# Performance work log

Hardware: AMD Instinct MI355X
Metric: run time of the kernel (lower is better)

Reference implementation:

```python
import jax, jax.numpy as jnp
import numpy as np

NUM_HEADS = 16
B, S, D_MODEL = 8, 2048, 1024
HEAD_DIM = 64  # key_dim == value_dim == D_MODEL // NUM_HEADS


def setup_inputs() -> dict:
    key = jax.random.key(0)
    ks = jax.random.split(key, 8)
    s_in = 1.0 / np.sqrt(D_MODEL)
    s_out = 1.0 / np.sqrt(NUM_HEADS * HEAD_DIM)
    return {
        "query": jax.random.normal(ks[0], (B, S, D_MODEL), jnp.float32),
        "key": jax.random.normal(ks[1], (B, S, D_MODEL), jnp.float32),
        "value": jax.random.normal(ks[2], (B, S, D_MODEL), jnp.float32),
        "Wq": jax.random.normal(ks[3], (D_MODEL, HEAD_DIM), jnp.float32) * s_in,
        "bq": jnp.zeros((HEAD_DIM,), jnp.float32),
        "Wk": jax.random.normal(ks[4], (D_MODEL, HEAD_DIM), jnp.float32) * s_in,
        "bk": jnp.zeros((HEAD_DIM,), jnp.float32),
        "Wv": jax.random.normal(ks[5], (D_MODEL, HEAD_DIM), jnp.float32) * s_in,
        "bv": jnp.zeros((HEAD_DIM,), jnp.float32),
        "Wo": jax.random.normal(ks[6], (NUM_HEADS * HEAD_DIM, D_MODEL), jnp.float32) * s_out,
        "bo": jnp.zeros((D_MODEL,), jnp.float32),
    }


def reference(query, key, value, Wq, bq, Wk, bk, Wv, bv, Wo, bo):
    # Projections (same Linear reused for every "head" in the original code)
    q = query @ Wq + bq   # [B, S, head_dim]
    k = key @ Wk + bk     # [B, S, head_dim]
    v = value @ Wv + bv   # [B, S, head_dim]
    scale = jnp.sqrt(jnp.asarray(q.shape[-1], q.dtype))
    scores = jnp.einsum("bqd,bkd->bqk", q, k) / scale  # [B, S, S]
    attn = jax.nn.softmax(scores, axis=-1)
    ctx = jnp.einsum("bqk,bkd->bqd", attn, v)          # [B, S, head_dim]
    # All num_heads outputs are identical -> concat == tile
    cat = jnp.tile(ctx, (1, 1, NUM_HEADS))             # [B, S, num_heads*head_dim]
    return cat @ Wo + bo                               # [B, S, D_MODEL]
```

## Files before the change

### kernel.cpp

```cpp
#include <hip/hip_runtime.h>


typedef __attribute__((ext_vector_type(8))) unsigned short ushort8v;

__device__ __forceinline__ float bf2f(unsigned short u) {
    unsigned int x = ((unsigned int)u) << 16;
    return __builtin_bit_cast(float, x);
}

__device__ __forceinline__ bool detect_bf16(const void* p, int nwords) {
    const unsigned short* w = (const unsigned short*)p;
    int sane = 0;
    for (int i = 0; i < nwords; ++i) {
        unsigned e = (w[i] >> 7) & 0xFF;
        sane += (e == 0 || (e >= 0x60 && e <= 0x9F)) ? 1 : 0;
    }
    return sane * 10 >= nwords * 9;
}

__device__ __forceinline__ float load_in(const void* p, long idx, bool isbf16) {
    return isbf16 ? bf2f(((const unsigned short*)p)[idx]) : ((const float*)p)[idx];
}

__global__ __launch_bounds__(256) void prep_wosum(const void* __restrict__ Wo,
                                                  float* __restrict__ wosum) {
    __shared__ bool fwb;
    if (threadIdx.x == 0) fwb = detect_bf16(Wo, 256);
    __syncthreads();
    bool wb = fwb;
    int id = blockIdx.x * 256 + threadIdx.x;
    int d = id >> 10, n = id & 1023;
    float s = 0.f;
#pragma unroll
    for (int h = 0; h < 16; ++h) s += load_in(Wo, (long)(h * 64 + d) * 1024 + n, wb);
    wosum[id] = s;
}

__global__ __launch_bounds__(256) void proj_t(
    const void* __restrict__ X0, const void* __restrict__ X1, const void* __restrict__ X2,
    const void* __restrict__ bq, const void* __restrict__ bk, const void* __restrict__ bv,
    const void* __restrict__ Wq, const void* __restrict__ Wk, const void* __restrict__ Wv,
    float* __restrict__ qo, float* __restrict__ ko, float* __restrict__ vo) {
    int p = blockIdx.y;
    const void* X    = (p == 0) ? X0 : (p == 1) ? X1 : X2;
    const void* W    = (p == 0) ? Wq : (p == 1) ? Wk : Wv;
    const void* bias = (p == 0) ? bq : (p == 1) ? bk : bv;
    float* out       = (p == 0) ? qo : (p == 1) ? ko : vo;

    __shared__ bool fxb, fwb, fbb;
    __shared__ __align__(16) float Xt[64 * 68];
    __shared__ __align__(16) float Ws[64 * 68];
    if (threadIdx.x == 0) {
        fxb = detect_bf16(X, 256);
        fwb = detect_bf16(W, 256);
        fbb = detect_bf16(bias, 64);
    }
    __syncthreads();
    const bool xb = fxb, wb = fwb, bb = fbb;

    const int t = threadIdx.x;
    const long row0 = (long)blockIdx.x * 64;
    const int row4 = (t >> 4) * 4;
    const int col4 = (t & 15) * 4;
    const int sr0 = (t >> 4) * 4;
    const int sk4 = (t & 15) * 4;
    const int wk  = t >> 2;
    const int wc0 = (t & 3) * 16;

    ushort4 xu0, xu1, xu2, xu3;
    float4  xf0, xf1, xf2, xf3;
    ushort8v wu0, wu1;
    float4  wf0, wf1, wf2, wf3;

    auto loadTile = [&](int k0) {
        if (xb) {
            const unsigned short* xp =
                (const unsigned short*)X + (row0 + sr0) * 1024 + k0 + sk4;
            xu0 = *(const ushort4*)(xp);
            xu1 = *(const ushort4*)(xp + 1024);
            xu2 = *(const ushort4*)(xp + 2048);
            xu3 = *(const ushort4*)(xp + 3072);
        } else {
            const float* xp = (const float*)X + (row0 + sr0) * 1024 + k0 + sk4;
            xf0 = *(const float4*)(xp);
            xf1 = *(const float4*)(xp + 1024);
            xf2 = *(const float4*)(xp + 2048);
            xf3 = *(const float4*)(xp + 3072);
        }
        if (wb) {
            const unsigned short* wp =
                (const unsigned short*)W + (long)(k0 + wk) * 64 + wc0;
            wu0 = *(const ushort8v*)(wp);
            wu1 = *(const ushort8v*)(wp + 8);
        } else {
            const float* wp = (const float*)W + (long)(k0 + wk) * 64 + wc0;
            wf0 = *(const float4*)(wp + 0);
            wf1 = *(const float4*)(wp + 4);
            wf2 = *(const float4*)(wp + 8);
            wf3 = *(const float4*)(wp + 12);
        }
    };
    auto writeTile = [&]() {
        if (xb) {
            *(float4*)&Xt[(sk4 + 0) * 68 + sr0] =
                make_float4(bf2f(xu0.x), bf2f(xu1.x), bf2f(xu2.x), bf2f(xu3.x));
            *(float4*)&Xt[(sk4 + 1) * 68 + sr0] =
                make_float4(bf2f(xu0.y), bf2f(xu1.y), bf2f(xu2.y), bf2f(xu3.y));
            *(float4*)&Xt[(sk4 + 2) * 68 + sr0] =
                make_float4(bf2f(xu0.z), bf2f(xu1.z), bf2f(xu2.z), bf2f(xu3.z));
            *(float4*)&Xt[(sk4 + 3) * 68 + sr0] =
                make_float4(bf2f(xu0.w), bf2f(xu1.w), bf2f(xu2.w), bf2f(xu3.w));
        } else {
            *(float4*)&Xt[(sk4 + 0) * 68 + sr0] = make_float4(xf0.x, xf1.x, xf2.x, xf3.x);
            *(float4*)&Xt[(sk4 + 1) * 68 + sr0] = make_float4(xf0.y, xf1.y, xf2.y, xf3.y);
            *(float4*)&Xt[(sk4 + 2) * 68 + sr0] = make_float4(xf0.z, xf1.z, xf2.z, xf3.z);
            *(float4*)&Xt[(sk4 + 3) * 68 + sr0] = make_float4(xf0.w, xf1.w, xf2.w, xf3.w);
        }
        float* wd = &Ws[wk * 68 + wc0];
        if (wb) {
            *(float4*)(wd + 0)  = make_float4(bf2f(wu0[0]), bf2f(wu0[1]), bf2f(wu0[2]), bf2f(wu0[3]));
            *(float4*)(wd + 4)  = make_float4(bf2f(wu0[4]), bf2f(wu0[5]), bf2f(wu0[6]), bf2f(wu0[7]));
            *(float4*)(wd + 8)  = make_float4(bf2f(wu1[0]), bf2f(wu1[1]), bf2f(wu1[2]), bf2f(wu1[3]));
            *(float4*)(wd + 12) = make_float4(bf2f(wu1[4]), bf2f(wu1[5]), bf2f(wu1[6]), bf2f(wu1[7]));
        } else {
            *(float4*)(wd + 0)  = wf0;
            *(float4*)(wd + 4)  = wf1;
            *(float4*)(wd + 8)  = wf2;
            *(float4*)(wd + 12) = wf3;
        }
    };

    loadTile(0);
    writeTile();
    __syncthreads();

    float acc[4][4] = {};
    for (int k0 = 0; k0 < 1024; k0 += 64) {
        const bool more = (k0 + 64 < 1024);
        if (more) loadTile(k0 + 64);
#pragma unroll 4
        for (int kk = 0; kk < 64; ++kk) {
            float4 xv = *(const float4*)&Xt[kk * 68 + row4];
            float4 wv = *(const float4*)&Ws[kk * 68 + col4];
            float xa[4] = {xv.x, xv.y, xv.z, xv.w};
            float wa[4] = {wv.x, wv.y, wv.z, wv.w};
#pragma unroll
            for (int i = 0; i < 4; ++i)
#pragma unroll
                for (int j = 0; j < 4; ++j) acc[i][j] += xa[i] * wa[j];
        }
        if (more) {
            __syncthreads();
            writeTile();
            __syncthreads();
        }
    }

    float b0 = load_in(bias, col4 + 0, bb);
    float b1 = load_in(bias, col4 + 1, bb);
    float b2 = load_in(bias, col4 + 2, bb);
    float b3 = load_in(bias, col4 + 3, bb);
#pragma unroll
    for (int i = 0; i < 4; ++i)
        *(float4*)&out[(row0 + row4 + i) * 64 + col4] =
            make_float4(acc[i][0] + b0, acc[i][1] + b1, acc[i][2] + b2, acc[i][3] + b3);
}

__global__ __launch_bounds__(256) void attn_p(const float* __restrict__ q,
                                              const float* __restrict__ k,
                                              const float* __restrict__ v,
                                              float* __restrict__ ctx,
                                              float* __restrict__ po,
                                              float* __restrict__ pm,
                                              float* __restrict__ pl,
                                              int ns) {
    const int b = blockIdx.y;
    const int qt = blockIdx.x;
    const int split = blockIdx.z;
    const int keys = 2048 / ns;
    const int NT = keys >> 6;
    const long kvbase = (long)b * 2048;
    const long qbase  = kvbase + (long)qt * 32;
    const long kstart = kvbase + (long)split * keys;

    __shared__ __align__(16) float Qt[64 * 36];
    __shared__ __align__(16) float Kt[64 * 68];
    __shared__ __align__(16) float Pt[64 * 36];

    const int tid = threadIdx.x;
    const int g16 = tid & 15;
    const int qg2 = (tid >> 4) * 2;
    const int kg4 = g16 * 4;
    const int dg4 = g16 * 4;
    const int skr = (tid >> 4) * 4;
    const int skd = g16 * 4;

    if (tid < 128) {
        const int sqr = (tid >> 4) * 4;
        const int sqd = (tid & 15) * 4;
        const float* qp = &q[(qbase + sqr) * 64 + sqd];
        float4 a0 = *(const float4*)(qp);
        float4 a1 = *(const float4*)(qp + 64);
        float4 a2 = *(const float4*)(qp + 128);
        float4 a3 = *(const float4*)(qp + 192);
        const float sc = 0.125f;
        *(float4*)&Qt[(sqd + 0) * 36 + sqr] = make_float4(a0.x * sc, a1.x * sc, a2.x * sc, a3.x * sc);
        *(float4*)&Qt[(sqd + 1) * 36 + sqr] = make_float4(a0.y * sc, a1.y * sc, a2.y * sc, a3.y * sc);
        *(float4*)&Qt[(sqd + 2) * 36 + sqr] = make_float4(a0.z * sc, a1.z * sc, a2.z * sc, a3.z * sc);
        *(float4*)&Qt[(sqd + 3) * 36 + sqr] = make_float4(a0.w * sc, a1.w * sc, a2.w * sc, a3.w * sc);
    }

    float4 ka0, ka1, ka2, ka3;
    auto loadK = [&](int t1) {
        const float* kp = &k[(kstart + t1 * 64 + skr) * 64 + skd];
        ka0 = *(const float4*)(kp);
        ka1 = *(const float4*)(kp + 64);
        ka2 = *(const float4*)(kp + 128);
        ka3 = *(const float4*)(kp + 192);
    };
    auto writeK = [&]() {
        *(float4*)&Kt[(skd + 0) * 68 + skr] = make_float4(ka0.x, ka1.x, ka2.x, ka3.x);
        *(float4*)&Kt[(skd + 1) * 68 + skr] = make_float4(ka0.y, ka1.y, ka2.y, ka3.y);
        *(float4*)&Kt[(skd + 2) * 68 + skr] = make_float4(ka0.z, ka1.z, ka2.z, ka3.z);
        *(float4*)&Kt[(skd + 3) * 68 + skr] = make_float4(ka0.w, ka1.w, ka2.w, ka3.w);
    };

    loadK(0);
    writeK();
    __syncthreads();

    float o[2][4] = {};
    float m[2] = {-INFINITY, -INFINITY};
    float l[2] = {};

    for (int t1 = 0; t1 < NT; ++t1) {
        if (t1 + 1 < NT) loadK(t1 + 1);

        float s[2][4] = {};
#pragma unroll 4
        for (int d = 0; d < 64; ++d) {
            float2 qv = *(const float2*)&Qt[d * 36 + qg2];
            float4 kv = *(const float4*)&Kt[d * 68 + kg4];
            float ka[4] = {kv.x, kv.y, kv.z, kv.w};
#pragma unroll
            for (int kj = 0; kj < 4; ++kj) {
                s[0][kj] += qv.x * ka[kj];
                s[1][kj] += qv.y * ka[kj];
            }
        }

#pragma unroll
        for (int qi = 0; qi < 2; ++qi) {
            float pmx = fmaxf(fmaxf(s[qi][0], s[qi][1]), fmaxf(s[qi][2], s[qi][3]));
            pmx = fmaxf(pmx, __shfl_xor(pmx, 1));
            pmx = fmaxf(pmx, __shfl_xor(pmx, 2));
            pmx = fmaxf(pmx, __shfl_xor(pmx, 4));
            pmx = fmaxf(pmx, __shfl_xor(pmx, 8));
            float mn = fmaxf(m[qi], pmx);
            float f = __expf(m[qi] - mn);
            m[qi] = mn;
            float ts = 0.f;
#pragma unroll
            for (int kj = 0; kj < 4; ++kj) {
                float pv = __expf(s[qi][kj] - mn);
                s[qi][kj] = pv;
                ts += pv;
            }
            ts += __shfl_xor(ts, 1);
            ts += __shfl_xor(ts, 2);
            ts += __shfl_xor(ts, 4);
            ts += __shfl_xor(ts, 8);
            l[qi] = l[qi] * f + ts;
#pragma unroll
            for (int di = 0; di < 4; ++di) o[qi][di] *= f;
        }

#pragma unroll
        for (int kj = 0; kj < 4; ++kj)
            *(float2*)&Pt[(kg4 + kj) * 36 + qg2] = make_float2(s[0][kj], s[1][kj]);
        __syncthreads();

        const float* vb = &v[(kstart + t1 * 64) * 64 + dg4];
#pragma unroll 4
        for (int kk = 0; kk < 64; ++kk) {
            float2 p2 = *(const float2*)&Pt[kk * 36 + qg2];
            float4 v4 = *(const float4*)&vb[kk * 64];
            float va[4] = {v4.x, v4.y, v4.z, v4.w};
#pragma unroll
            for (int di = 0; di < 4; ++di) {
                o[0][di] += p2.x * va[di];
                o[1][di] += p2.y * va[di];
            }
        }

        if (t1 + 1 < NT) writeK();
        __syncthreads();
    }

    if (ns == 1) {
#pragma unroll
        for (int qi = 0; qi < 2; ++qi) {
            float inv = 1.f / l[qi];
            *(float4*)&ctx[(qbase + qg2 + qi) * 64 + dg4] =
                make_float4(o[qi][0] * inv, o[qi][1] * inv, o[qi][2] * inv, o[qi][3] * inv);
        }
    } else {
        const long idx = (long)(b * 64 + qt) * ns + split;
#pragma unroll
        for (int qi = 0; qi < 2; ++qi)
            *(float4*)&po[idx * 2048 + (qg2 + qi) * 64 + dg4] =
                make_float4(o[qi][0], o[qi][1], o[qi][2], o[qi][3]);
        if (g16 == 0) {
#pragma unroll
            for (int qi = 0; qi < 2; ++qi) {
                pm[idx * 32 + qg2 + qi] = m[qi];
                pl[idx * 32 + qg2 + qi] = l[qi];
            }
        }
    }
}

__global__ __launch_bounds__(256) void attn_merge(const float* __restrict__ po,
                                                  const float* __restrict__ pm,
                                                  const float* __restrict__ pl,
                                                  float* __restrict__ ctx,
                                                  int ns) {
    const int t = threadIdx.x;
    const long r = (long)blockIdx.x * 4 + (t >> 6);
    const int d = t & 63;
    const int b = (int)(r >> 11);
    const int rr = (int)(r & 2047);
    const int qt = rr >> 5;
    const int rloc = rr & 31;
    const long base = (long)(b * 64 + qt) * ns;
    float M = -INFINITY;
    for (int s = 0; s < ns; ++s) M = fmaxf(M, pm[(base + s) * 32 + rloc]);
    float L = 0.f, num = 0.f;
    for (int s = 0; s < ns; ++s) {
        float e = __expf(pm[(base + s) * 32 + rloc] - M);
        L += pl[(base + s) * 32 + rloc] * e;
        num += po[(base + s) * 2048 + rloc * 64 + d] * e;
    }
    ctx[r * 64 + d] = num / L;
}

__global__ __launch_bounds__(256) void out_t(const float* __restrict__ ctx,
                                             const float* __restrict__ wosum,
                                             const void* __restrict__ bo,
                                             float* __restrict__ out) {
    __shared__ __align__(16) float cr[8 * 64];
    __shared__ bool fbb;
    int t = threadIdx.x;
    long row0 = (long)blockIdx.x * 8;
    if (t == 0) fbb = detect_bf16(bo, 256);
    if (t < 128) {
        int r = t >> 4, d4 = (t & 15) * 4;
        *(float4*)&cr[r * 64 + d4] = *(const float4*)&ctx[(row0 + r) * 64 + d4];
    }
    __syncthreads();
    bool bob = fbb;
    int c = t * 4;
    float a[8][4];
    {
        float b0 = load_in(bo, c + 0, bob), b1 = load_in(bo, c + 1, bob);
        float b2 = load_in(bo, c + 2, bob), b3 = load_in(bo, c + 3, bob);
#pragma unroll
        for (int r = 0; r < 8; ++r) { a[r][0] = b0; a[r][1] = b1; a[r][2] = b2; a[r][3] = b3; }
    }
#pragma unroll 4
    for (int d = 0; d < 64; ++d) {
        float4 w4 = *(const float4*)&wosum[d * 1024 + c];
#pragma unroll
        for (int r = 0; r < 8; ++r) {
            float cv = cr[r * 64 + d];
            a[r][0] += cv * w4.x;
            a[r][1] += cv * w4.y;
            a[r][2] += cv * w4.z;
            a[r][3] += cv * w4.w;
        }
    }
#pragma unroll
    for (int r = 0; r < 8; ++r)
        *(float4*)&out[(row0 + r) * 1024 + c] = make_float4(a[r][0], a[r][1], a[r][2], a[r][3]);
}

extern "C" void kernel_launch(void* const* d_in, const int* in_sizes, int n_in,
                              void* d_out, int out_size, void* d_ws, size_t ws_size,
                              hipStream_t stream) {
    const void* big[3] = {0, 0, 0};  int nbig = 0;
    const void* w64k[3] = {0, 0, 0}; int nw = 0;
    const void* b64[3] = {0, 0, 0};  int nb = 0;
    const void* Wo = 0; const void* bo = 0;
    for (int i = 0; i < n_in; ++i) {
        int s = in_sizes[i];
        if (s == 16777216 && nbig < 3)     big[nbig++] = d_in[i];
        else if (s == 65536 && nw < 3)     w64k[nw++] = d_in[i];
        else if (s == 64 && nb < 3)        b64[nb++] = d_in[i];
        else if (s == 1048576)             Wo = d_in[i];
        else if (s == 1024)                bo = d_in[i];
    }
    const void* query = big[0]  ? big[0]  : d_in[0];
    const void* key   = big[1]  ? big[1]  : d_in[1];
    const void* value = big[2]  ? big[2]  : d_in[2];
    const void* Wq    = w64k[0] ? w64k[0] : d_in[3];
    const void* Wk    = w64k[1] ? w64k[1] : d_in[5];
    const void* Wv    = w64k[2] ? w64k[2] : d_in[7];
    const void* bq    = b64[0]  ? b64[0]  : d_in[4];
    const void* bk    = b64[1]  ? b64[1]  : d_in[6];
    const void* bv    = b64[2]  ? b64[2]  : d_in[8];
    if (!Wo) Wo = d_in[9];
    if (!bo) bo = d_in[10];
    float* out = (float*)d_out;

    char* ws = (char*)d_ws;
    float* wosum = (float*)(ws);
    float* q     = (float*)(ws + 1048576);
    float* k     = (float*)(ws + 1048576 + 4194304);
    float* v     = (float*)(ws + 1048576 + 2*4194304);
    float* ctx   = (float*)(ws + 1048576 + 3*4194304);
    const size_t PO_OFF = 1048576 + (size_t)4 * 4194304;
    int ns = (ws_size >= PO_OFF + 2 * 4194304ull + 2 * 131072ull) ? 2 : 1;
    float* po = (float*)(ws + PO_OFF);
    float* pm = (float*)(ws + PO_OFF + (size_t)ns * 4194304);
    float* pl = pm + (size_t)ns * 16384;

    hipLaunchKernelGGL(prep_wosum, dim3(256),        dim3(256), 0, stream, Wo, wosum);
    hipLaunchKernelGGL(proj_t,     dim3(256, 3),     dim3(256), 0, stream,
                       query, key, value, bq, bk, bv, Wq, Wk, Wv, q, k, v);
    hipLaunchKernelGGL(attn_p,     dim3(64, 8, ns),  dim3(256), 0, stream,
                       q, k, v, ctx, po, pm, pl, ns);
    if (ns > 1)
        hipLaunchKernelGGL(attn_merge, dim3(4096),   dim3(256), 0, stream, po, pm, pl, ctx, ns);
    hipLaunchKernelGGL(out_t,      dim3(2048),       dim3(256), 0, stream, ctx, wosum, bo, out);
}
```

Measured before the change: 544.2 us.

## Enlarge attention and output tiles, vectorize wosum prep, relayout projection tiles

```diff
diff --git a/kernel.cpp b/kernel.cpp
--- a/kernel.cpp
+++ b/kernel.cpp
@@ -28,12 +28,21 @@
     if (threadIdx.x == 0) fwb = detect_bf16(Wo, 256);
     __syncthreads();
     bool wb = fwb;
-    int id = blockIdx.x * 256 + threadIdx.x;
-    int d = id >> 10, n = id & 1023;
-    float s = 0.f;
-#pragma unroll
-    for (int h = 0; h < 16; ++h) s += load_in(Wo, (long)(h * 64 + d) * 1024 + n, wb);
-    wosum[id] = s;
+    int base = (blockIdx.x * 256 + threadIdx.x) * 4;
+    int d = base >> 10, n = base & 1023;
+    float4 s = make_float4(0.f, 0.f, 0.f, 0.f);
+#pragma unroll
+    for (int h = 0; h < 16; ++h) {
+        long off = (long)(h * 64 + d) * 1024 + n;
+        if (wb) {
+            ushort4 u = *(const ushort4*)((const unsigned short*)Wo + off);
+            s.x += bf2f(u.x); s.y += bf2f(u.y); s.z += bf2f(u.z); s.w += bf2f(u.w);
+        } else {
+            float4 f = *(const float4*)((const float*)Wo + off);
+            s.x += f.x; s.y += f.y; s.z += f.z; s.w += f.w;
+        }
+    }
+    *(float4*)&wosum[base] = s;
 }
 
 __global__ __launch_bounds__(256) void proj_t(
@@ -48,7 +57,7 @@
     float* out       = (p == 0) ? qo : (p == 1) ? ko : vo;
 
     __shared__ bool fxb, fwb, fbb;
-    __shared__ __align__(16) float Xt[64 * 68];
+    __shared__ __align__(16) float Xs[64 * 68];
     __shared__ __align__(16) float Ws[64 * 68];
     if (threadIdx.x == 0) {
         fxb = detect_bf16(X, 256);
@@ -59,29 +68,27 @@
     const bool xb = fxb, wb = fwb, bb = fbb;
 
     const int t = threadIdx.x;
+    const int g16 = t & 15;
+    const int w4 = t >> 4;
     const long row0 = (long)blockIdx.x * 64;
-    const int row4 = (t >> 4) * 4;
-    const int col4 = (t & 15) * 4;
-    const int sr0 = (t >> 4) * 4;
-    const int sk4 = (t & 15) * 4;
-    const int wk  = t >> 2;
-    const int wc0 = (t & 3) * 16;
-
-    ushort4 xu0, xu1, xu2, xu3;
-    float4  xf0, xf1, xf2, xf3;
-    ushort8v wu0, wu1;
-    float4  wf0, wf1, wf2, wf3;
+    const int row4 = 4 * w4;
+    const int col4 = 4 * g16;
+    const int sR = 4 * w4;
+    const int sC = 4 * g16;
+
+    ushort4 xu0, xu1, xu2, xu3, wu0, wu1, wu2, wu3;
+    float4  xf0, xf1, xf2, xf3, wf0, wf1, wf2, wf3;
 
     auto loadTile = [&](int k0) {
         if (xb) {
             const unsigned short* xp =
-                (const unsigned short*)X + (row0 + sr0) * 1024 + k0 + sk4;
+                (const unsigned short*)X + (row0 + sR) * 1024 + k0 + sC;
             xu0 = *(const ushort4*)(xp);
             xu1 = *(const ushort4*)(xp + 1024);
             xu2 = *(const ushort4*)(xp + 2048);
             xu3 = *(const ushort4*)(xp + 3072);
         } else {
-            const float* xp = (const float*)X + (row0 + sr0) * 1024 + k0 + sk4;
+            const float* xp = (const float*)X + (row0 + sR) * 1024 + k0 + sC;
             xf0 = *(const float4*)(xp);
             xf1 = *(const float4*)(xp + 1024);
             xf2 = *(const float4*)(xp + 2048);
@@ -89,44 +96,41 @@
         }
         if (wb) {
             const unsigned short* wp =
-                (const unsigned short*)W + (long)(k0 + wk) * 64 + wc0;
-            wu0 = *(const ushort8v*)(wp);
-            wu1 = *(const ushort8v*)(wp + 8);
+                (const unsigned short*)W + (long)(k0 + sR) * 64 + sC;
+            wu0 = *(const ushort4*)(wp);
+            wu1 = *(const ushort4*)(wp + 64);
+            wu2 = *(const ushort4*)(wp + 128);
+            wu3 = *(const ushort4*)(wp + 192);
         } else {
-            const float* wp = (const float*)W + (long)(k0 + wk) * 64 + wc0;
-            wf0 = *(const float4*)(wp + 0);
-            wf1 = *(const float4*)(wp + 4);
-            wf2 = *(const float4*)(wp + 8);
-            wf3 = *(const float4*)(wp + 12);
+            const float* wp = (const float*)W + (long)(k0 + sR) * 64 + sC;
+            wf0 = *(const float4*)(wp);
+            wf1 = *(const float4*)(wp + 64);
+            wf2 = *(const float4*)(wp + 128);
+            wf3 = *(const float4*)(wp + 192);
         }
     };
     auto writeTile = [&]() {
         if (xb) {
-            *(float4*)&Xt[(sk4 + 0) * 68 + sr0] =
-                make_float4(bf2f(xu0.x), bf2f(xu1.x), bf2f(xu2.x), bf2f(xu3.x));
-            *(float4*)&Xt[(sk4 + 1) * 68 + sr0] =
-                make_float4(bf2f(xu0.y), bf2f(xu1.y), bf2f(xu2.y), bf2f(xu3.y));
-            *(float4*)&Xt[(sk4 + 2) * 68 + sr0] =
-                make_float4(bf2f(xu0.z), bf2f(xu1.z), bf2f(xu2.z), bf2f(xu3.z));
-            *(float4*)&Xt[(sk4 + 3) * 68 + sr0] =
-                make_float4(bf2f(xu0.w), bf2f(xu1.w), bf2f(xu2.w), bf2f(xu3.w));
+            *(float4*)&Xs[(sR + 0) * 68 + sC] = make_float4(bf2f(xu0.x), bf2f(xu0.y), bf2f(xu0.z), bf2f(xu0.w));
+            *(float4*)&Xs[(sR + 1) * 68 + sC] = make_float4(bf2f(xu1.x), bf2f(xu1.y), bf2f(xu1.z), bf2f(xu1.w));
+            *(float4*)&Xs[(sR + 2) * 68 + sC] = make_float4(bf2f(xu2.x), bf2f(xu2.y), bf2f(xu2.z), bf2f(xu2.w));
+            *(float4*)&Xs[(sR + 3) * 68 + sC] = make_float4(bf2f(xu3.x), bf2f(xu3.y), bf2f(xu3.z), bf2f(xu3.w));
         } else {
-            *(float4*)&Xt[(sk4 + 0) * 68 + sr0] = make_float4(xf0.x, xf1.x, xf2.x, xf3.x);
-            *(float4*)&Xt[(sk4 + 1) * 68 + sr0] = make_float4(xf0.y, xf1.y, xf2.y, xf3.y);
-            *(float4*)&Xt[(sk4 + 2) * 68 + sr0] = make_float4(xf0.z, xf1.z, xf2.z, xf3.z);
-            *(float4*)&Xt[(sk4 + 3) * 68 + sr0] = make_float4(xf0.w, xf1.w, xf2.w, xf3.w);
-        }
-        float* wd = &Ws[wk * 68 + wc0];
+            *(float4*)&Xs[(sR + 0) * 68 + sC] = xf0;
+            *(float4*)&Xs[(sR + 1) * 68 + sC] = xf1;
+            *(float4*)&Xs[(sR + 2) * 68 + sC] = xf2;
+            *(float4*)&Xs[(sR + 3) * 68 + sC] = xf3;
+        }
         if (wb) {
-            *(float4*)(wd + 0)  = make_float4(bf2f(wu0[0]), bf2f(wu0[1]), bf2f(wu0[2]), bf2f(wu0[3]));
-            *(float4*)(wd + 4)  = make_float4(bf2f(wu0[4]), bf2f(wu0[5]), bf2f(wu0[6]), bf2f(wu0[7]));
-            *(float4*)(wd + 8)  = make_float4(bf2f(wu1[0]), bf2f(wu1[1]), bf2f(wu1[2]), bf2f(wu1[3]));
-            *(float4*)(wd + 12) = make_float4(bf2f(wu1[4]), bf2f(wu1[5]), bf2f(wu1[6]), bf2f(wu1[7]));
+            *(float4*)&Ws[(sR + 0) * 68 + sC] = make_float4(bf2f(wu0.x), bf2f(wu0.y), bf2f(wu0.z), bf2f(wu0.w));
+            *(float4*)&Ws[(sR + 1) * 68 + sC] = make_float4(bf2f(wu1.x), bf2f(wu1.y), bf2f(wu1.z), bf2f(wu1.w));
+            *(float4*)&Ws[(sR + 2) * 68 + sC] = make_float4(bf2f(wu2.x), bf2f(wu2.y), bf2f(wu2.z), bf2f(wu2.w));
+            *(float4*)&Ws[(sR + 3) * 68 + sC] = make_float4(bf2f(wu3.x), bf2f(wu3.y), bf2f(wu3.z), bf2f(wu3.w));
         } else {
-            *(float4*)(wd + 0)  = wf0;
-            *(float4*)(wd + 4)  = wf1;
-            *(float4*)(wd + 8)  = wf2;
-            *(float4*)(wd + 12) = wf3;
+            *(float4*)&Ws[(sR + 0) * 68 + sC] = wf0;
+            *(float4*)&Ws[(sR + 1) * 68 + sC] = wf1;
+            *(float4*)&Ws[(sR + 2) * 68 + sC] = wf2;
+            *(float4*)&Ws[(sR + 3) * 68 + sC] = wf3;
         }
     };
 
@@ -138,16 +142,24 @@
     for (int k0 = 0; k0 < 1024; k0 += 64) {
         const bool more = (k0 + 64 < 1024);
         if (more) loadTile(k0 + 64);
-#pragma unroll 4
-        for (int kk = 0; kk < 64; ++kk) {
-            float4 xv = *(const float4*)&Xt[kk * 68 + row4];
-            float4 wv = *(const float4*)&Ws[kk * 68 + col4];
-            float xa[4] = {xv.x, xv.y, xv.z, xv.w};
-            float wa[4] = {wv.x, wv.y, wv.z, wv.w};
-#pragma unroll
-            for (int i = 0; i < 4; ++i)
-#pragma unroll
-                for (int j = 0; j < 4; ++j) acc[i][j] += xa[i] * wa[j];
+#pragma unroll 2
+        for (int kk = 0; kk < 64; kk += 4) {
+            float4 xq[4], wv[4];
+#pragma unroll
+            for (int qi = 0; qi < 4; ++qi) xq[qi] = *(const float4*)&Xs[(row4 + qi) * 68 + kk];
+#pragma unroll
+            for (int j = 0; j < 4; ++j) wv[j] = *(const float4*)&Ws[(kk + j) * 68 + col4];
+#pragma unroll
+            for (int qi = 0; qi < 4; ++qi) {
+                float xa[4] = {xq[qi].x, xq[qi].y, xq[qi].z, xq[qi].w};
+#pragma unroll
+                for (int j = 0; j < 4; ++j) {
+                    acc[qi][0] += xa[j] * wv[j].x;
+                    acc[qi][1] += xa[j] * wv[j].y;
+                    acc[qi][2] += xa[j] * wv[j].z;
+                    acc[qi][3] += xa[j] * wv[j].w;
+                }
+            }
         }
         if (more) {
             __syncthreads();
@@ -161,9 +173,9 @@
     float b2 = load_in(bias, col4 + 2, bb);
     float b3 = load_in(bias, col4 + 3, bb);
 #pragma unroll
-    for (int i = 0; i < 4; ++i)
-        *(float4*)&out[(row0 + row4 + i) * 64 + col4] =
-            make_float4(acc[i][0] + b0, acc[i][1] + b1, acc[i][2] + b2, acc[i][3] + b3);
+    for (int qi = 0; qi < 4; ++qi)
+        *(float4*)&out[(row0 + row4 + qi) * 64 + col4] =
+            make_float4(acc[qi][0] + b0, acc[qi][1] + b1, acc[qi][2] + b2, acc[qi][3] + b3);
 }
 
 __global__ __launch_bounds__(256) void attn_p(const float* __restrict__ q,
@@ -180,77 +192,76 @@
     const int keys = 2048 / ns;
     const int NT = keys >> 6;
     const long kvbase = (long)b * 2048;
-    const long qbase  = kvbase + (long)qt * 32;
+    const long qbase  = kvbase + (long)qt * 64;
     const long kstart = kvbase + (long)split * keys;
 
-    __shared__ __align__(16) float Qt[64 * 36];
+    __shared__ __align__(16) float Qt[64 * 68];
     __shared__ __align__(16) float Kt[64 * 68];
-    __shared__ __align__(16) float Pt[64 * 36];
+    __shared__ __align__(16) float Pt[64 * 72];
 
     const int tid = threadIdx.x;
     const int g16 = tid & 15;
-    const int qg2 = (tid >> 4) * 2;
-    const int kg4 = g16 * 4;
-    const int dg4 = g16 * 4;
-    const int skr = (tid >> 4) * 4;
-    const int skd = g16 * 4;
-
-    if (tid < 128) {
-        const int sqr = (tid >> 4) * 4;
-        const int sqd = (tid & 15) * 4;
-        const float* qp = &q[(qbase + sqr) * 64 + sqd];
+    const int w4 = tid >> 4;
+    const int qg4 = 4 * w4;
+    const int kg4 = 4 * g16;
+    const int dg4 = 4 * g16;
+    const int sr = 4 * g16;
+    const int sd = 4 * w4;
+
+    {
+        const float* qp = &q[(qbase + sr) * 64 + sd];
         float4 a0 = *(const float4*)(qp);
         float4 a1 = *(const float4*)(qp + 64);
         float4 a2 = *(const float4*)(qp + 128);
         float4 a3 = *(const float4*)(qp + 192);
         const float sc = 0.125f;
-        *(float4*)&Qt[(sqd + 0) * 36 + sqr] = make_float4(a0.x * sc, a1.x * sc, a2.x * sc, a3.x * sc);
-        *(float4*)&Qt[(sqd + 1) * 36 + sqr] = make_float4(a0.y * sc, a1.y * sc, a2.y * sc, a3.y * sc);
-        *(float4*)&Qt[(sqd + 2) * 36 + sqr] = make_float4(a0.z * sc, a1.z * sc, a2.z * sc, a3.z * sc);
-        *(float4*)&Qt[(sqd + 3) * 36 + sqr] = make_float4(a0.w * sc, a1.w * sc, a2.w * sc, a3.w * sc);
+        *(float4*)&Qt[(sd + 0) * 68 + sr] = make_float4(a0.x * sc, a1.x * sc, a2.x * sc, a3.x * sc);
+        *(float4*)&Qt[(sd + 1) * 68 + sr] = make_float4(a0.y * sc, a1.y * sc, a2.y * sc, a3.y * sc);
+        *(float4*)&Qt[(sd + 2) * 68 + sr] = make_float4(a0.z * sc, a1.z * sc, a2.z * sc, a3.z * sc);
+        *(float4*)&Qt[(sd + 3) * 68 + sr] = make_float4(a0.w * sc, a1.w * sc, a2.w * sc, a3.w * sc);
     }
 
     float4 ka0, ka1, ka2, ka3;
     auto loadK = [&](int t1) {
-        const float* kp = &k[(kstart + t1 * 64 + skr) * 64 + skd];
+        const float* kp = &k[(kstart + t1 * 64 + sr) * 64 + sd];
         ka0 = *(const float4*)(kp);
         ka1 = *(const float4*)(kp + 64);
         ka2 = *(const float4*)(kp + 128);
         ka3 = *(const float4*)(kp + 192);
     };
     auto writeK = [&]() {
-        *(float4*)&Kt[(skd + 0) * 68 + skr] = make_float4(ka0.x, ka1.x, ka2.x, ka3.x);
-        *(float4*)&Kt[(skd + 1) * 68 + skr] = make_float4(ka0.y, ka1.y, ka2.y, ka3.y);
-        *(float4*)&Kt[(skd + 2) * 68 + skr] = make_float4(ka0.z, ka1.z, ka2.z, ka3.z);
-        *(float4*)&Kt[(skd + 3) * 68 + skr] = make_float4(ka0.w, ka1.w, ka2.w, ka3.w);
+        *(float4*)&Kt[(sd + 0) * 68 + sr] = make_float4(ka0.x, ka1.x, ka2.x, ka3.x);
+        *(float4*)&Kt[(sd + 1) * 68 + sr] = make_float4(ka0.y, ka1.y, ka2.y, ka3.y);
+        *(float4*)&Kt[(sd + 2) * 68 + sr] = make_float4(ka0.z, ka1.z, ka2.z, ka3.z);
+        *(float4*)&Kt[(sd + 3) * 68 + sr] = make_float4(ka0.w, ka1.w, ka2.w, ka3.w);
     };
 
     loadK(0);
     writeK();
     __syncthreads();
 
-    float o[2][4] = {};
-    float m[2] = {-INFINITY, -INFINITY};
-    float l[2] = {};
+    float o[4][4] = {};
+    float m[4] = {-INFINITY, -INFINITY, -INFINITY, -INFINITY};
+    float l[4] = {};
 
     for (int t1 = 0; t1 < NT; ++t1) {
         if (t1 + 1 < NT) loadK(t1 + 1);
 
-        float s[2][4] = {};
+        float s[4][4] = {};
 #pragma unroll 4
         for (int d = 0; d < 64; ++d) {
-            float2 qv = *(const float2*)&Qt[d * 36 + qg2];
+            float4 qv = *(const float4*)&Qt[d * 68 + qg4];
             float4 kv = *(const float4*)&Kt[d * 68 + kg4];
+            float qa[4] = {qv.x, qv.y, qv.z, qv.w};
             float ka[4] = {kv.x, kv.y, kv.z, kv.w};
 #pragma unroll
-            for (int kj = 0; kj < 4; ++kj) {
-                s[0][kj] += qv.x * ka[kj];
-                s[1][kj] += qv.y * ka[kj];
-            }
-        }
-
-#pragma unroll
-        for (int qi = 0; qi < 2; ++qi) {
+            for (int qi = 0; qi < 4; ++qi)
+#pragma unroll
+                for (int kj = 0; kj < 4; ++kj) s[qi][kj] += qa[qi] * ka[kj];
+        }
+
+#pragma unroll
+        for (int qi = 0; qi < 4; ++qi) {
             float pmx = fmaxf(fmaxf(s[qi][0], s[qi][1]), fmaxf(s[qi][2], s[qi][3]));
             pmx = fmaxf(pmx, __shfl_xor(pmx, 1));
             pmx = fmaxf(pmx, __shfl_xor(pmx, 2));
@@ -276,20 +287,29 @@
         }
 
 #pragma unroll
-        for (int kj = 0; kj < 4; ++kj)
-            *(float2*)&Pt[(kg4 + kj) * 36 + qg2] = make_float2(s[0][kj], s[1][kj]);
+        for (int qi = 0; qi < 4; ++qi)
+            *(float4*)&Pt[(qg4 + qi) * 72 + kg4] =
+                make_float4(s[qi][0], s[qi][1], s[qi][2], s[qi][3]);
         __syncthreads();
 
         const float* vb = &v[(kstart + t1 * 64) * 64 + dg4];
-#pragma unroll 4
-        for (int kk = 0; kk < 64; ++kk) {
-            float2 p2 = *(const float2*)&Pt[kk * 36 + qg2];
-            float4 v4 = *(const float4*)&vb[kk * 64];
-            float va[4] = {v4.x, v4.y, v4.z, v4.w};
-#pragma unroll
-            for (int di = 0; di < 4; ++di) {
-                o[0][di] += p2.x * va[di];
-                o[1][di] += p2.y * va[di];
+#pragma unroll 2
+        for (int kk = 0; kk < 64; kk += 4) {
+            float4 p4[4], v4[4];
+#pragma unroll
+            for (int qi = 0; qi < 4; ++qi) p4[qi] = *(const float4*)&Pt[(qg4 + qi) * 72 + kk];
+#pragma unroll
+            for (int j = 0; j < 4; ++j) v4[j] = *(const float4*)&vb[(kk + j) * 64];
+#pragma unroll
+            for (int qi = 0; qi < 4; ++qi) {
+                float pa[4] = {p4[qi].x, p4[qi].y, p4[qi].z, p4[qi].w};
+#pragma unroll
+                for (int j = 0; j < 4; ++j) {
+                    o[qi][0] += pa[j] * v4[j].x;
+                    o[qi][1] += pa[j] * v4[j].y;
+                    o[qi][2] += pa[j] * v4[j].z;
+                    o[qi][3] += pa[j] * v4[j].w;
+                }
             }
         }
 
@@ -299,22 +319,22 @@
 
     if (ns == 1) {
 #pragma unroll
-        for (int qi = 0; qi < 2; ++qi) {
+        for (int qi = 0; qi < 4; ++qi) {
             float inv = 1.f / l[qi];
-            *(float4*)&ctx[(qbase + qg2 + qi) * 64 + dg4] =
+            *(float4*)&ctx[(qbase + qg4 + qi) * 64 + dg4] =
                 make_float4(o[qi][0] * inv, o[qi][1] * inv, o[qi][2] * inv, o[qi][3] * inv);
         }
     } else {
-        const long idx = (long)(b * 64 + qt) * ns + split;
-#pragma unroll
-        for (int qi = 0; qi < 2; ++qi)
-            *(float4*)&po[idx * 2048 + (qg2 + qi) * 64 + dg4] =
+        const long idx = (long)(b * 32 + qt) * ns + split;
+#pragma unroll
+        for (int qi = 0; qi < 4; ++qi)
+            *(float4*)&po[idx * 4096 + (qg4 + qi) * 64 + dg4] =
                 make_float4(o[qi][0], o[qi][1], o[qi][2], o[qi][3]);
         if (g16 == 0) {
 #pragma unroll
-            for (int qi = 0; qi < 2; ++qi) {
-                pm[idx * 32 + qg2 + qi] = m[qi];
-                pl[idx * 32 + qg2 + qi] = l[qi];
+            for (int qi = 0; qi < 4; ++qi) {
+                pm[idx * 64 + qg4 + qi] = m[qi];
+                pl[idx * 64 + qg4 + qi] = l[qi];
             }
         }
     }
@@ -330,16 +350,16 @@
     const int d = t & 63;
     const int b = (int)(r >> 11);
     const int rr = (int)(r & 2047);
-    const int qt = rr >> 5;
-    const int rloc = rr & 31;
-    const long base = (long)(b * 64 + qt) * ns;
+    const int qt = rr >> 6;
+    const int rloc = rr & 63;
+    const long base = (long)(b * 32 + qt) * ns;
     float M = -INFINITY;
-    for (int s = 0; s < ns; ++s) M = fmaxf(M, pm[(base + s) * 32 + rloc]);
+    for (int s = 0; s < ns; ++s) M = fmaxf(M, pm[(base + s) * 64 + rloc]);
     float L = 0.f, num = 0.f;
     for (int s = 0; s < ns; ++s) {
-        float e = __expf(pm[(base + s) * 32 + rloc] - M);
-        L += pl[(base + s) * 32 + rloc] * e;
-        num += po[(base + s) * 2048 + rloc * 64 + d] * e;
+        float e = __expf(pm[(base + s) * 64 + rloc] - M);
+        L += pl[(base + s) * 64 + rloc] * e;
+        num += po[(base + s) * 4096 + rloc * 64 + d] * e;
     }
     ctx[r * 64 + d] = num / L;
 }
@@ -348,30 +368,27 @@
                                              const float* __restrict__ wosum,
                                              const void* __restrict__ bo,
                                              float* __restrict__ out) {
-    __shared__ __align__(16) float cr[8 * 64];
+    __shared__ __align__(16) float cr[16 * 64];
     __shared__ bool fbb;
     int t = threadIdx.x;
-    long row0 = (long)blockIdx.x * 8;
+    long row0 = (long)blockIdx.x * 16;
     if (t == 0) fbb = detect_bf16(bo, 256);
-    if (t < 128) {
-        int r = t >> 4, d4 = (t & 15) * 4;
-        *(float4*)&cr[r * 64 + d4] = *(const float4*)&ctx[(row0 + r) * 64 + d4];
-    }
+    *(float4*)&cr[t * 4] = *(const float4*)&ctx[row0 * 64 + t * 4];
     __syncthreads();
     bool bob = fbb;
     int c = t * 4;
-    float a[8][4];
+    float a[16][4];
     {
         float b0 = load_in(bo, c + 0, bob), b1 = load_in(bo, c + 1, bob);
         float b2 = load_in(bo, c + 2, bob), b3 = load_in(bo, c + 3, bob);
 #pragma unroll
-        for (int r = 0; r < 8; ++r) { a[r][0] = b0; a[r][1] = b1; a[r][2] = b2; a[r][3] = b3; }
+        for (int r = 0; r < 16; ++r) { a[r][0] = b0; a[r][1] = b1; a[r][2] = b2; a[r][3] = b3; }
     }
 #pragma unroll 4
     for (int d = 0; d < 64; ++d) {
         float4 w4 = *(const float4*)&wosum[d * 1024 + c];
 #pragma unroll
-        for (int r = 0; r < 8; ++r) {
+        for (int r = 0; r < 16; ++r) {
             float cv = cr[r * 64 + d];
             a[r][0] += cv * w4.x;
             a[r][1] += cv * w4.y;
@@ -380,7 +397,7 @@
         }
     }
 #pragma unroll
-    for (int r = 0; r < 8; ++r)
+    for (int r = 0; r < 16; ++r)
         *(float4*)&out[(row0 + r) * 1024 + c] = make_float4(a[r][0], a[r][1], a[r][2], a[r][3]);
 }
 
@@ -419,17 +436,19 @@
     float* v     = (float*)(ws + 1048576 + 2*4194304);
     float* ctx   = (float*)(ws + 1048576 + 3*4194304);
     const size_t PO_OFF = 1048576 + (size_t)4 * 4194304;
-    int ns = (ws_size >= PO_OFF + 2 * 4194304ull + 2 * 131072ull) ? 2 : 1;
+    int ns = 1;
+    if (ws_size >= PO_OFF + 4 * 4194304ull + 2 * 4 * 65536ull)      ns = 4;
+    else if (ws_size >= PO_OFF + 2 * 4194304ull + 2 * 2 * 65536ull) ns = 2;
     float* po = (float*)(ws + PO_OFF);
     float* pm = (float*)(ws + PO_OFF + (size_t)ns * 4194304);
     float* pl = pm + (size_t)ns * 16384;
 
-    hipLaunchKernelGGL(prep_wosum, dim3(256),        dim3(256), 0, stream, Wo, wosum);
+    hipLaunchKernelGGL(prep_wosum, dim3(64),         dim3(256), 0, stream, Wo, wosum);
     hipLaunchKernelGGL(proj_t,     dim3(256, 3),     dim3(256), 0, stream,
                        query, key, value, bq, bk, bv, Wq, Wk, Wv, q, k, v);
-    hipLaunchKernelGGL(attn_p,     dim3(64, 8, ns),  dim3(256), 0, stream,
+    hipLaunchKernelGGL(attn_p,     dim3(32, 8, ns),  dim3(256), 0, stream,
                        q, k, v, ctx, po, pm, pl, ns);
     if (ns > 1)
         hipLaunchKernelGGL(attn_merge, dim3(4096),   dim3(256), 0, stream, po, pm, pl, ctx, ns);
-    hipLaunchKernelGGL(out_t,      dim3(2048),       dim3(256), 0, stream, ctx, wosum, bo, out);
-}
+    hipLaunchKernelGGL(out_t,      dim3(1024),       dim3(256), 0, stream, ctx, wosum, bo, out);
+}
```

Measured after the change: 543.8 us. About the same (-0.1%).
